# Performance work log

Measured on AMD Instinct MI355X. Metric: run time of the kernel, lower is better.

Reference implementation:

```python
import jax, jax.numpy as jnp
import numpy as np

N, E, D, H, C, L = 50000, 600000, 128, 128, 40, 2
NEG_SLOPE = 0.1


def setup_inputs() -> dict:
    key = jax.random.key(0)
    ks = jax.random.split(key, 12)

    def lin(k, din, dout):
        return (jax.random.normal(k, (din, dout), jnp.float32) / np.sqrt(din)).astype(jnp.float32)

    x = jax.random.normal(ks[0], (N, D), jnp.float32)
    edge_index = jax.random.randint(ks[1], (2, E), 0, N, dtype=jnp.int32)
    return {
        "x": x,
        "edge_index": edge_index,
        "enc_Wl": lin(ks[2], D, H),
        "enc_Wr": lin(ks[3], D, H),
        "enc_b": jnp.zeros((H,), jnp.float32),
        "lay_Wl": jnp.stack([lin(jax.random.fold_in(ks[4], i), H, H) for i in range(L)]),
        "lay_Wr": jnp.stack([lin(jax.random.fold_in(ks[5], i), H, H) for i in range(L)]),
        "lay_b": jnp.zeros((L, H), jnp.float32),
        "dec_Wl": lin(ks[6], H, C),
        "dec_Wr": lin(ks[7], H, C),
        "dec_b": jnp.zeros((C,), jnp.float32),
    }


def _sage(x, src, dst, inv_cnt, Wl, Wr, b):
    # mean-aggregate neighbor messages: gather x[src], scatter-sum to dst, divide by degree
    agg = jax.ops.segment_sum(x[src], dst, num_segments=N) * inv_cnt  # [N, d_in]
    return agg @ Wl + x @ Wr + b


def reference(x, edge_index, enc_Wl, enc_Wr, enc_b, lay_Wl, lay_Wr, lay_b, dec_Wl, dec_Wr, dec_b):
    src, dst = edge_index[0], edge_index[1]
    # in-degree per target node, clamped to 1 (PyG scatter-mean semantics: isolated nodes get 0)
    deg = jax.ops.segment_sum(jnp.ones((E,), jnp.float32), dst, num_segments=N)
    inv_cnt = (1.0 / jnp.maximum(deg, 1.0))[:, None]  # [N, 1]

    h = jax.nn.leaky_relu(_sage(x, src, dst, inv_cnt, enc_Wl, enc_Wr, enc_b), NEG_SLOPE)
    for i in range(L):
        h = jax.nn.leaky_relu(_sage(h, src, dst, inv_cnt, lay_Wl[i], lay_Wr[i], lay_b[i]), NEG_SLOPE)
    out = _sage(h, src, dst, inv_cnt, dec_Wl, dec_Wr, dec_b)
    return jax.nn.log_softmax(out, axis=1)
```

## Files before the change

kernel.cpp:

```cpp
#include <hip/hip_runtime.h>
#include <hip/hip_bf16.h>

#define NN 50000
#define EE 600000
#define HH 128
#define CC 40
#define NEG 0.1f
#define CAP 40
#define NSLOT 50176
#define NBLK (NSLOT / 16)

typedef __attribute__((ext_vector_type(8))) short bf16x8;
typedef __attribute__((ext_vector_type(4))) float f32x4;

__device__ __forceinline__ unsigned short f2bf(float f) {
    unsigned u = __float_as_uint(f);
    unsigned r = u + 0x7fffu + ((u >> 16) & 1u);
    return (unsigned short)(r >> 16);
}
__device__ __forceinline__ float bfhi(unsigned v) { return __uint_as_float(v & 0xFFFF0000u); }
__device__ __forceinline__ float bflo(unsigned v) { return __uint_as_float(v << 16); }

__global__ void k_build(const int* __restrict__ src, const int* __restrict__ dst,
                        int* __restrict__ counts, int* __restrict__ csr) {
    int e = blockIdx.x * blockDim.x + threadIdx.x;
    if (e < EE) {
        int d = dst[e];
        if ((unsigned)d < (unsigned)NN) {
            int sl = atomicAdd(&counts[d], 1);
            if (sl < CAP) csr[d * CAP + sl] = src[e];
        }
    }
}

__global__ void k_hist(const int* __restrict__ counts, int* __restrict__ hist) {
    __shared__ int lh[16];
    if (threadIdx.x < 16) lh[threadIdx.x] = 0;
    __syncthreads();
    int n = blockIdx.x * 256 + threadIdx.x;
    if (n < NN) {
        int c = counts[n]; c = c < CAP ? c : CAP;
        atomicAdd(&lh[(c + 3) >> 2], 1);
    }
    __syncthreads();
    if (threadIdx.x < 11) atomicAdd(&hist[threadIdx.x], lh[threadIdx.x]);
}

__global__ void k_prefix(const int* __restrict__ hist, int* __restrict__ base) {
    if (threadIdx.x == 0) {
        int acc = 0;
        for (int r = 10; r >= 0; --r) {
            base[r] = acc;
            acc += (hist[r] + 15) & ~15;
        }
    }
}

__global__ void k_place(const int* __restrict__ counts, const int* __restrict__ base,
                        int* __restrict__ fill, unsigned* __restrict__ perm) {
    __shared__ int lcnt[16];
    __shared__ int lbase[16];
    int t = threadIdx.x;
    if (t < 16) lcnt[t] = 0;
    __syncthreads();
    int n = blockIdx.x * 256 + t;
    int r = 0, lslot = 0, c = 0;
    if (n < NN) {
        c = counts[n]; c = c < CAP ? c : CAP;
        r = (c + 3) >> 2;
        lslot = atomicAdd(&lcnt[r], 1);
    }
    __syncthreads();
    if (t < 11 && lcnt[t] > 0) lbase[t] = atomicAdd(&fill[t], lcnt[t]);
    __syncthreads();
    if (n < NN) {
        int slot = base[r] + lbase[r] + lslot;
        if (slot >= 0 && slot < NSLOT) perm[slot] = (unsigned)n | ((unsigned)c << 16);
    }
}

struct PrepArgs {
    const float* wsrc[8];
    unsigned short* wdst[8];
    int* counts;
    const float* x;
    unsigned* xb;
    unsigned* perm;
    int* aux;
};

template <int DOUT, int DOUTP>
__device__ __forceinline__ void swz_one(const float* __restrict__ W,
                                        unsigned short* __restrict__ dstf, int idx) {
    int k = idx / DOUTP, n = idx % DOUTP;
    unsigned short val = (n < DOUT) ? f2bf(W[k * DOUT + n]) : (unsigned short)0;
    int kt = k >> 5, kin = k & 31, nt = n >> 4, nin = n & 15;
    int lane = ((kin >> 3) << 4) | nin;
    int j = kin & 7;
    int NT = DOUTP >> 4;
    dstf[(((kt * NT + nt) * 64) + lane) * 8 + j] = val;
}

#define XCB ((NN * HH / 4 + 255) / 256)
#define PFB ((NSLOT + 255) / 256)

__global__ void k_prep(PrepArgs a) {
    int b = blockIdx.x;
    if (b < 384) {
        int tid = b * 256 + threadIdx.x;
        if (tid < NN) a.counts[tid] = 0;
        int which = b >> 6;
        int idx = (b & 63) * 256 + threadIdx.x;
        swz_one<HH, HH>(a.wsrc[which], a.wdst[which], idx);
    } else if (b < 432) {
        int bb = b - 384;
        int which = 6 + bb / 24;
        int idx = (bb % 24) * 256 + threadIdx.x;
        swz_one<CC, 48>(a.wsrc[which], a.wdst[which], idx);
    } else if (b < 432 + XCB) {
        int t = (b - 432) * 256 + threadIdx.x;
        if (t < NN * HH / 4) {
            float4 v = ((const float4*)a.x)[t];
            uint2 o;
            o.x = ((unsigned)f2bf(v.y) << 16) | f2bf(v.x);
            o.y = ((unsigned)f2bf(v.w) << 16) | f2bf(v.z);
            ((uint2*)a.xb)[t] = o;
        }
    } else {
        int i = (b - (432 + XCB)) * 256 + threadIdx.x;
        if (i < NSLOT) a.perm[i] = 0xFFFFFFFFu;
        if (i < 64) a.aux[i] = 0;
    }
}

template <int R>
__device__ __forceinline__ void gather_batch(const int* __restrict__ crow,
                                             const uint4* __restrict__ hw4,
                                             int s, int gg, int cnt, int base_r,
                                             float (&acc)[8]) {
    int rv[R]; uint4 vb[R];
#pragma unroll
    for (int r = 0; r < R; ++r) rv[r] = crow[(base_r + r) * 4 + s];
#pragma unroll
    for (int r = 0; r < R; ++r) {
        unsigned rw = ((unsigned)rv[r] < (unsigned)NN) ? (unsigned)rv[r] : 0u;
        vb[r] = hw4[(size_t)rw * 16 + gg];
    }
#pragma unroll
    for (int r = 0; r < R; ++r) {
        if ((base_r + r) * 4 + s < cnt) {
            acc[0] += bflo(vb[r].x); acc[1] += bfhi(vb[r].x);
            acc[2] += bflo(vb[r].y); acc[3] += bfhi(vb[r].y);
            acc[4] += bflo(vb[r].z); acc[5] += bfhi(vb[r].z);
            acc[6] += bflo(vb[r].w); acc[7] += bfhi(vb[r].w);
        }
    }
}

template <int MODE>
__global__ __launch_bounds__(1024, 8) void k_layer(
    const unsigned short* __restrict__ hin,
    const unsigned* __restrict__ perm,
    const int* __restrict__ csr,
    const unsigned short* __restrict__ B1f, const unsigned short* __restrict__ B2f,
    const float* __restrict__ bias, unsigned short* __restrict__ out,
    const unsigned short* __restrict__ Tf, unsigned short* __restrict__ tOut) {
    __shared__ unsigned lds[16][72];
    __shared__ int nodeTab[16];
    int wid = threadIdx.x >> 6;
    int lane = threadIdx.x & 63;
    int m0 = blockIdx.x * 16;
    int gg = lane & 15;
    int s = lane >> 4;
    const uint4* hw4 = (const uint4*)hin;

    unsigned pe = perm[m0 + wid];
    int pes = __builtin_amdgcn_readfirstlane((int)pe);
    int node = pes & 0xffff;
    int cnt = (pes >> 16) & 0xffff;
    int valid = node < NN;
    if (lane == 0) nodeTab[wid] = valid ? node : (1 << 30);
    int rounds = valid ? (cnt + 3) >> 2 : 0;
    rounds = rounds < 10 ? rounds : 10;
    float sc = 1.0f / (float)((valid && cnt > 0) ? cnt : 1);
    const int* crow = csr + (size_t)(valid ? node : 0) * CAP;

    float acc[8];
#pragma unroll
    for (int d = 0; d < 8; ++d) acc[d] = 0.f;

    switch (rounds) {
        case 0: break;
        case 1: gather_batch<1>(crow, hw4, s, gg, cnt, 0, acc); break;
        case 2: gather_batch<2>(crow, hw4, s, gg, cnt, 0, acc); break;
        case 3: gather_batch<3>(crow, hw4, s, gg, cnt, 0, acc); break;
        case 4: gather_batch<4>(crow, hw4, s, gg, cnt, 0, acc); break;
        case 5: gather_batch<5>(crow, hw4, s, gg, cnt, 0, acc); break;
        case 6: gather_batch<3>(crow, hw4, s, gg, cnt, 0, acc);
                gather_batch<3>(crow, hw4, s, gg, cnt, 3, acc); break;
        case 7: gather_batch<4>(crow, hw4, s, gg, cnt, 0, acc);
                gather_batch<3>(crow, hw4, s, gg, cnt, 4, acc); break;
        case 8: gather_batch<4>(crow, hw4, s, gg, cnt, 0, acc);
                gather_batch<4>(crow, hw4, s, gg, cnt, 4, acc); break;
        case 9: gather_batch<5>(crow, hw4, s, gg, cnt, 0, acc);
                gather_batch<4>(crow, hw4, s, gg, cnt, 5, acc); break;
        default: gather_batch<5>(crow, hw4, s, gg, cnt, 0, acc);
                 gather_batch<5>(crow, hw4, s, gg, cnt, 5, acc); break;
    }

#pragma unroll
    for (int d = 0; d < 8; ++d) {
        float t = acc[d];
        t += __shfl_xor(t, 16, 64);
        t += __shfl_xor(t, 32, 64);
        acc[d] = t * sc;
    }
    if (lane < 16) {
        uint4 w4;
        w4.x = ((unsigned)f2bf(acc[1]) << 16) | f2bf(acc[0]);
        w4.y = ((unsigned)f2bf(acc[3]) << 16) | f2bf(acc[2]);
        w4.z = ((unsigned)f2bf(acc[5]) << 16) | f2bf(acc[4]);
        w4.w = ((unsigned)f2bf(acc[7]) << 16) | f2bf(acc[6]);
        *(uint4*)&lds[wid][gg * 4] = w4;
    }
    __syncthreads();

    int nin = lane & 15;
    int kq = lane >> 4;
    unsigned short hv[4];

    if (wid < 8) {
        const unsigned* arow = &lds[nin][0];
        int node2 = nodeTab[nin];
        int na = node2 < NN ? node2 : 0;
        f32x4 acc1 = (f32x4){0.f, 0.f, 0.f, 0.f};

#pragma unroll
        for (int kt = 0; kt < 4; ++kt) {
            bf16x8 a1 = *(const bf16x8*)(arow + kt * 16 + kq * 4);
            bf16x8 a2 = *(const bf16x8*)(hin + (size_t)na * HH + kt * 32 + kq * 8);
            bf16x8 b1 = *(const bf16x8*)(B1f + (((kt * 8 + wid) * 64) + lane) * 8);
            acc1 = __builtin_amdgcn_mfma_f32_16x16x32_bf16(a1, b1, acc1, 0, 0, 0);
            bf16x8 b2 = *(const bf16x8*)(B2f + (((kt * 8 + wid) * 64) + lane) * 8);
            acc1 = __builtin_amdgcn_mfma_f32_16x16x32_bf16(a2, b2, acc1, 0, 0, 0);
        }

        int col = wid * 16 + nin;
        float bv = bias[col];
#pragma unroll
        for (int r = 0; r < 4; ++r) {
            float v = acc1[r] + bv;
            v = fmaxf(v, NEG * v);
            hv[r] = f2bf(v);
            int nm = nodeTab[kq * 4 + r];
            if (nm < NN) out[(size_t)nm * HH + col] = hv[r];
        }
    }

    if (MODE == 1) {
        __syncthreads();
        unsigned short* lsh = (unsigned short*)&lds[0][0];
        if (wid < 8) {
            int col = wid * 16 + nin;
#pragma unroll
            for (int r = 0; r < 4; ++r) lsh[(kq * 4 + r) * 144 + col] = hv[r];
        }
        __syncthreads();
        if (wid < 3) {
            f32x4 at = (f32x4){0.f, 0.f, 0.f, 0.f};
#pragma unroll
            for (int kt = 0; kt < 4; ++kt) {
                bf16x8 a = *(const bf16x8*)&lsh[nin * 144 + kt * 32 + kq * 8];
                bf16x8 b = *(const bf16x8*)(Tf + (((kt * 3 + wid) * 64) + lane) * 8);
                at = __builtin_amdgcn_mfma_f32_16x16x32_bf16(a, b, at, 0, 0, 0);
            }
#pragma unroll
            for (int r = 0; r < 4; ++r) {
                int nm = nodeTab[kq * 4 + r];
                if (nm < NN) tOut[(size_t)nm * 48 + wid * 16 + nin] = f2bf(at[r]);
            }
        }
    }
}

template <int R>
__device__ __forceinline__ void gatherd_batch(const int* __restrict__ crow,
                                              const uint4* __restrict__ t4,
                                              int s, int g6, int cnt, float (&acc)[8]) {
    int rv[R]; uint4 vb[R];
#pragma unroll
    for (int r = 0; r < R; ++r) rv[r] = crow[r * 8 + s];
#pragma unroll
    for (int r = 0; r < R; ++r) {
        unsigned rw = ((unsigned)rv[r] < (unsigned)NN) ? (unsigned)rv[r] : 0u;
        vb[r] = t4[(size_t)rw * 6 + g6];
    }
#pragma unroll
    for (int r = 0; r < R; ++r) {
        if (r * 8 + s < cnt) {
            acc[0] += bflo(vb[r].x); acc[1] += bfhi(vb[r].x);
            acc[2] += bflo(vb[r].y); acc[3] += bfhi(vb[r].y);
            acc[4] += bflo(vb[r].z); acc[5] += bfhi(vb[r].z);
            acc[6] += bflo(vb[r].w); acc[7] += bfhi(vb[r].w);
        }
    }
}

__global__ __launch_bounds__(1024, 8) void k_dec(
    const unsigned short* __restrict__ tbuf,
    const unsigned short* __restrict__ h1,
    const unsigned* __restrict__ perm,
    const int* __restrict__ csr,
    const unsigned short* __restrict__ B2f, const float* __restrict__ bias,
    float* __restrict__ out) {
    __shared__ float aggT[16][52];
    __shared__ int nodeTab[16];
    int wid = threadIdx.x >> 6;
    int lane = threadIdx.x & 63;
    int m0 = blockIdx.x * 16;
    int g = lane & 7;
    int g6 = g < 6 ? g : g - 6;
    int s = lane >> 3;
    const uint4* t4 = (const uint4*)tbuf;

    unsigned pe = perm[m0 + wid];
    int pes = __builtin_amdgcn_readfirstlane((int)pe);
    int node = pes & 0xffff;
    int cnt = (pes >> 16) & 0xffff;
    int valid = node < NN;
    if (lane == 0) nodeTab[wid] = valid ? node : (1 << 30);
    int rounds = valid ? (cnt + 7) >> 3 : 0;
    rounds = rounds < 5 ? rounds : 5;
    float sc = 1.0f / (float)((valid && cnt > 0) ? cnt : 1);
    const int* crow = csr + (size_t)(valid ? node : 0) * CAP;

    float acc[8];
#pragma unroll
    for (int d = 0; d < 8; ++d) acc[d] = 0.f;

    switch (rounds) {
        case 0: break;
        case 1: gatherd_batch<1>(crow, t4, s, g6, cnt, acc); break;
        case 2: gatherd_batch<2>(crow, t4, s, g6, cnt, acc); break;
        case 3: gatherd_batch<3>(crow, t4, s, g6, cnt, acc); break;
        case 4: gatherd_batch<4>(crow, t4, s, g6, cnt, acc); break;
        default: gatherd_batch<5>(crow, t4, s, g6, cnt, acc); break;
    }

#pragma unroll
    for (int d = 0; d < 8; ++d) {
        float t = acc[d];
        t += __shfl_xor(t, 8, 64);
        t += __shfl_xor(t, 16, 64);
        t += __shfl_xor(t, 32, 64);
        acc[d] = t * sc;
    }
    if (s == 0 && g < 6) {
        float4 p0, p1;
        p0.x = acc[0]; p0.y = acc[1]; p0.z = acc[2]; p0.w = acc[3];
        p1.x = acc[4]; p1.y = acc[5]; p1.z = acc[6]; p1.w = acc[7];
        *(float4*)&aggT[wid][8 * g] = p0;
        *(float4*)&aggT[wid][8 * g + 4] = p1;
    }
    __syncthreads();
    if (wid != 0) return;

    int nin = lane & 15, kq = lane >> 4;
    int node2 = nodeTab[nin];
    int na = node2 < NN ? node2 : 0;
    f32x4 acc2[3];
#pragma unroll
    for (int j = 0; j < 3; ++j) acc2[j] = (f32x4){0.f, 0.f, 0.f, 0.f};
#pragma unroll
    for (int kt = 0; kt < 4; ++kt) {
        bf16x8 a2 = *(const bf16x8*)(h1 + (size_t)na * HH + kt * 32 + kq * 8);
#pragma unroll
        for (int j = 0; j < 3; ++j) {
            bf16x8 b2 = *(const bf16x8*)(B2f + (((kt * 3 + j) * 64) + lane) * 8);
            acc2[j] = __builtin_amdgcn_mfma_f32_16x16x32_bf16(a2, b2, acc2[j], 0, 0, 0);
        }
    }
    float bv[3];
#pragma unroll
    for (int t = 0; t < 3; ++t) {
        int col = t * 16 + nin;
        bv[t] = (col < CC) ? bias[col] : 0.f;
    }
#pragma unroll
    for (int r = 0; r < 4; ++r) {
        int ml = kq * 4 + r;
        int nm = nodeTab[ml];
        float v[3];
        float mx = -1e30f;
#pragma unroll
        for (int t = 0; t < 3; ++t) {
            int col = t * 16 + nin;
            v[t] = acc2[t][r] + aggT[ml][col] + bv[t];
            if (col < CC) mx = fmaxf(mx, v[t]);
        }
        for (int off = 1; off < 16; off <<= 1) mx = fmaxf(mx, __shfl_xor(mx, off, 64));
        float sm = 0.f;
#pragma unroll
        for (int t = 0; t < 3; ++t) {
            int col = t * 16 + nin;
            if (col < CC) sm += expf(v[t] - mx);
        }
        for (int off = 1; off < 16; off <<= 1) sm += __shfl_xor(sm, off, 64);
        float lse = mx + logf(sm);
#pragma unroll
        for (int t = 0; t < 3; ++t) {
            int col = t * 16 + nin;
            if (col < CC && nm < NN) out[(size_t)nm * CC + col] = v[t] - lse;
        }
    }
}

extern "C" void kernel_launch(void* const* d_in, const int* in_sizes, int n_in,
                              void* d_out, int out_size, void* d_ws, size_t ws_size,
                              hipStream_t stream) {
    const float* x      = (const float*)d_in[0];
    const int*   ei     = (const int*)d_in[1];
    const float* enc_Wl = (const float*)d_in[2];
    const float* enc_Wr = (const float*)d_in[3];
    const float* enc_b  = (const float*)d_in[4];
    const float* lay_Wl = (const float*)d_in[5];
    const float* lay_Wr = (const float*)d_in[6];
    const float* lay_b  = (const float*)d_in[7];
    const float* dec_Wl = (const float*)d_in[8];
    const float* dec_Wr = (const float*)d_in[9];
    const float* dec_b  = (const float*)d_in[10];
    float* out = (float*)d_out;

    const int* src = ei;
    const int* dst = ei + EE;

    char* p = (char*)d_ws;
    auto carve = [&](size_t bytes) {
        char* r = p;
        p += (bytes + 255) & ~(size_t)255;
        return r;
    };
    int*            counts = (int*)carve(NN * 4);
    int*            csr    = (int*)carve((size_t)NN * CAP * 4);
    unsigned short* h1     = (unsigned short*)carve((size_t)NN * HH * 2);
    unsigned short* h2     = (unsigned short*)carve((size_t)NN * HH * 2);
    unsigned short* tbuf   = (unsigned short*)carve((size_t)NN * 48 * 2 + 256);
    unsigned*       perm   = (unsigned*)carve((size_t)NSLOT * 4);
    int*            aux    = (int*)carve(64 * 4);
    unsigned short* wf[8];
    for (int i = 0; i < 6; ++i) wf[i] = (unsigned short*)carve(HH * HH * 2);
    wf[6] = (unsigned short*)carve(HH * 48 * 2);
    wf[7] = (unsigned short*)carve(HH * 48 * 2);

    {
        PrepArgs a;
        a.wsrc[0] = enc_Wl; a.wsrc[1] = enc_Wr;
        a.wsrc[2] = lay_Wl; a.wsrc[3] = lay_Wr;
        a.wsrc[4] = lay_Wl + HH * HH; a.wsrc[5] = lay_Wr + HH * HH;
        a.wsrc[6] = dec_Wl; a.wsrc[7] = dec_Wr;
        for (int i = 0; i < 8; ++i) a.wdst[i] = wf[i];
        a.counts = counts;
        a.x = x;
        a.xb = (unsigned*)h2;
        a.perm = perm;
        a.aux = aux;
        k_prep<<<432 + XCB + PFB, 256, 0, stream>>>(a);
    }

    k_build<<<(EE + 255) / 256, 256, 0, stream>>>(src, dst, counts, csr);
    k_hist<<<(NN + 255) / 256, 256, 0, stream>>>(counts, aux);
    k_prefix<<<1, 64, 0, stream>>>(aux, aux + 32);
    k_place<<<(NN + 255) / 256, 256, 0, stream>>>(counts, aux + 32, aux + 16, perm);

    k_layer<0><<<NBLK, 1024, 0, stream>>>(h2, perm, csr, wf[0], wf[1], enc_b,      h1, nullptr, nullptr);
    k_layer<0><<<NBLK, 1024, 0, stream>>>(h1, perm, csr, wf[2], wf[3], lay_b,      h2, nullptr, nullptr);
    k_layer<1><<<NBLK, 1024, 0, stream>>>(h2, perm, csr, wf[4], wf[5], lay_b + HH, h1, wf[6], tbuf);

    k_dec<<<NBLK, 1024, 0, stream>>>(tbuf, h1, perm, csr, wf[7], dec_b, out);
}
```

Before: 313.4 us.

## Store CSR neighbor indices as 16-bit and load rows with uniform wide loads

Neighbor indices in the padded CSR are stored as unsigned short instead of int, which halves the CSR footprint. Each wave now loads its whole 80-byte neighbor row as ten 64-bit loads from a wave-uniform address and extracts the 16-bit indices with shifts, replacing the per-lane scattered index loads. Feature-row gathers use nontemporal loads. This relies on node ids fitting in 16 bits (N=50000 does) and adds register pressure from holding ten 64-bit words per lane.

New measurement: 371.7 us. 1.19x slower.

```diff
diff --git a/kernel.cpp b/kernel.cpp
--- a/kernel.cpp
+++ b/kernel.cpp
@@ -12,6 +12,7 @@
 
 typedef __attribute__((ext_vector_type(8))) short bf16x8;
 typedef __attribute__((ext_vector_type(4))) float f32x4;
+typedef __attribute__((ext_vector_type(4))) unsigned uint4v;
 
 __device__ __forceinline__ unsigned short f2bf(float f) {
     unsigned u = __float_as_uint(f);
@@ -22,13 +23,13 @@
 __device__ __forceinline__ float bflo(unsigned v) { return __uint_as_float(v << 16); }
 
 __global__ void k_build(const int* __restrict__ src, const int* __restrict__ dst,
-                        int* __restrict__ counts, int* __restrict__ csr) {
+                        int* __restrict__ counts, unsigned short* __restrict__ csr) {
     int e = blockIdx.x * blockDim.x + threadIdx.x;
     if (e < EE) {
         int d = dst[e];
         if ((unsigned)d < (unsigned)NN) {
             int sl = atomicAdd(&counts[d], 1);
-            if (sl < CAP) csr[d * CAP + sl] = src[e];
+            if (sl < CAP) csr[d * CAP + sl] = (unsigned short)src[e];
         }
     }
 }
@@ -134,17 +135,18 @@
 }
 
 template <int R>
-__device__ __forceinline__ void gather_batch(const int* __restrict__ crow,
-                                             const uint4* __restrict__ hw4,
-                                             int s, int gg, int cnt, int base_r,
+__device__ __forceinline__ void gather_batch(const unsigned long long* cw,
+                                             const uint4v* __restrict__ hw4,
+                                             int s, int sh16, int gg, int cnt, int base_r,
                                              float (&acc)[8]) {
-    int rv[R]; uint4 vb[R];
-#pragma unroll
-    for (int r = 0; r < R; ++r) rv[r] = crow[(base_r + r) * 4 + s];
+    uint4v vb[R];
 #pragma unroll
     for (int r = 0; r < R; ++r) {
-        unsigned rw = ((unsigned)rv[r] < (unsigned)NN) ? (unsigned)rv[r] : 0u;
-        vb[r] = hw4[(size_t)rw * 16 + gg];
+        unsigned long long w = cw[base_r + r];
+        unsigned half = (s & 2) ? (unsigned)(w >> 32) : (unsigned)w;
+        unsigned idx = (half >> sh16) & 0xffffu;
+        idx = idx < (unsigned)NN ? idx : 0u;
+        vb[r] = __builtin_nontemporal_load(hw4 + (size_t)idx * 16 + gg);
     }
 #pragma unroll
     for (int r = 0; r < R; ++r) {
@@ -161,7 +163,7 @@
 __global__ __launch_bounds__(1024, 8) void k_layer(
     const unsigned short* __restrict__ hin,
     const unsigned* __restrict__ perm,
-    const int* __restrict__ csr,
+    const unsigned short* __restrict__ csr,
     const unsigned short* __restrict__ B1f, const unsigned short* __restrict__ B2f,
     const float* __restrict__ bias, unsigned short* __restrict__ out,
     const unsigned short* __restrict__ Tf, unsigned short* __restrict__ tOut) {
@@ -172,18 +174,24 @@
     int m0 = blockIdx.x * 16;
     int gg = lane & 15;
     int s = lane >> 4;
-    const uint4* hw4 = (const uint4*)hin;
-
-    unsigned pe = perm[m0 + wid];
-    int pes = __builtin_amdgcn_readfirstlane((int)pe);
-    int node = pes & 0xffff;
-    int cnt = (pes >> 16) & 0xffff;
+    int sh16 = (s & 1) * 16;
+    const uint4v* hw4 = (const uint4v*)hin;
+
+    int slot = __builtin_amdgcn_readfirstlane(m0 + wid);
+    unsigned pe = perm[slot];
+    int node = (int)(pe & 0xffffu);
+    int cnt = (int)((pe >> 16) & 0xffffu);
     int valid = node < NN;
     if (lane == 0) nodeTab[wid] = valid ? node : (1 << 30);
     int rounds = valid ? (cnt + 3) >> 2 : 0;
     rounds = rounds < 10 ? rounds : 10;
     float sc = 1.0f / (float)((valid && cnt > 0) ? cnt : 1);
-    const int* crow = csr + (size_t)(valid ? node : 0) * CAP;
+
+    const unsigned long long* cr8 =
+        (const unsigned long long*)(csr + (size_t)(valid ? node : 0) * CAP);
+    unsigned long long cw[10];
+#pragma unroll
+    for (int r = 0; r < 10; ++r) cw[r] = cr8[r];
 
     float acc[8];
 #pragma unroll
@@ -191,21 +199,21 @@
 
     switch (rounds) {
         case 0: break;
-        case 1: gather_batch<1>(crow, hw4, s, gg, cnt, 0, acc); break;
-        case 2: gather_batch<2>(crow, hw4, s, gg, cnt, 0, acc); break;
-        case 3: gather_batch<3>(crow, hw4, s, gg, cnt, 0, acc); break;
-        case 4: gather_batch<4>(crow, hw4, s, gg, cnt, 0, acc); break;
-        case 5: gather_batch<5>(crow, hw4, s, gg, cnt, 0, acc); break;
-        case 6: gather_batch<3>(crow, hw4, s, gg, cnt, 0, acc);
-                gather_batch<3>(crow, hw4, s, gg, cnt, 3, acc); break;
-        case 7: gather_batch<4>(crow, hw4, s, gg, cnt, 0, acc);
-                gather_batch<3>(crow, hw4, s, gg, cnt, 4, acc); break;
-        case 8: gather_batch<4>(crow, hw4, s, gg, cnt, 0, acc);
-                gather_batch<4>(crow, hw4, s, gg, cnt, 4, acc); break;
-        case 9: gather_batch<5>(crow, hw4, s, gg, cnt, 0, acc);
-                gather_batch<4>(crow, hw4, s, gg, cnt, 5, acc); break;
-        default: gather_batch<5>(crow, hw4, s, gg, cnt, 0, acc);
-                 gather_batch<5>(crow, hw4, s, gg, cnt, 5, acc); break;
+        case 1: gather_batch<1>(cw, hw4, s, sh16, gg, cnt, 0, acc); break;
+        case 2: gather_batch<2>(cw, hw4, s, sh16, gg, cnt, 0, acc); break;
+        case 3: gather_batch<3>(cw, hw4, s, sh16, gg, cnt, 0, acc); break;
+        case 4: gather_batch<4>(cw, hw4, s, sh16, gg, cnt, 0, acc); break;
+        case 5: gather_batch<5>(cw, hw4, s, sh16, gg, cnt, 0, acc); break;
+        case 6: gather_batch<3>(cw, hw4, s, sh16, gg, cnt, 0, acc);
+                gather_batch<3>(cw, hw4, s, sh16, gg, cnt, 3, acc); break;
+        case 7: gather_batch<4>(cw, hw4, s, sh16, gg, cnt, 0, acc);
+                gather_batch<3>(cw, hw4, s, sh16, gg, cnt, 4, acc); break;
+        case 8: gather_batch<4>(cw, hw4, s, sh16, gg, cnt, 0, acc);
+                gather_batch<4>(cw, hw4, s, sh16, gg, cnt, 4, acc); break;
+        case 9: gather_batch<5>(cw, hw4, s, sh16, gg, cnt, 0, acc);
+                gather_batch<4>(cw, hw4, s, sh16, gg, cnt, 5, acc); break;
+        default: gather_batch<5>(cw, hw4, s, sh16, gg, cnt, 0, acc);
+                 gather_batch<5>(cw, hw4, s, sh16, gg, cnt, 5, acc); break;
     }
 
 #pragma unroll
@@ -216,12 +224,12 @@
         acc[d] = t * sc;
     }
     if (lane < 16) {
-        uint4 w4;
-        w4.x = ((unsigned)f2bf(acc[1]) << 16) | f2bf(acc[0]);
-        w4.y = ((unsigned)f2bf(acc[3]) << 16) | f2bf(acc[2]);
-        w4.z = ((unsigned)f2bf(acc[5]) << 16) | f2bf(acc[4]);
-        w4.w = ((unsigned)f2bf(acc[7]) << 16) | f2bf(acc[6]);
-        *(uint4*)&lds[wid][gg * 4] = w4;
+        unsigned w4[4];
+        w4[0] = ((unsigned)f2bf(acc[1]) << 16) | f2bf(acc[0]);
+        w4[1] = ((unsigned)f2bf(acc[3]) << 16) | f2bf(acc[2]);
+        w4[2] = ((unsigned)f2bf(acc[5]) << 16) | f2bf(acc[4]);
+        w4[3] = ((unsigned)f2bf(acc[7]) << 16) | f2bf(acc[6]);
+        *(uint4v*)&lds[wid][gg * 4] = *(uint4v*)w4;
     }
     __syncthreads();
 
@@ -284,16 +292,18 @@
 }
 
 template <int R>
-__device__ __forceinline__ void gatherd_batch(const int* __restrict__ crow,
-                                              const uint4* __restrict__ t4,
-                                              int s, int g6, int cnt, float (&acc)[8]) {
-    int rv[R]; uint4 vb[R];
-#pragma unroll
-    for (int r = 0; r < R; ++r) rv[r] = crow[r * 8 + s];
+__device__ __forceinline__ void gatherd_batch(const unsigned long long* cw,
+                                              const uint4v* __restrict__ t4,
+                                              int s, int sh16, int g6, int cnt,
+                                              float (&acc)[8]) {
+    uint4v vb[R];
 #pragma unroll
     for (int r = 0; r < R; ++r) {
-        unsigned rw = ((unsigned)rv[r] < (unsigned)NN) ? (unsigned)rv[r] : 0u;
-        vb[r] = t4[(size_t)rw * 6 + g6];
+        unsigned long long w = (s & 4) ? cw[2 * r + 1] : cw[2 * r];
+        unsigned half = (s & 2) ? (unsigned)(w >> 32) : (unsigned)w;
+        unsigned idx = (half >> sh16) & 0xffffu;
+        idx = idx < (unsigned)NN ? idx : 0u;
+        vb[r] = __builtin_nontemporal_load(t4 + (size_t)idx * 6 + g6);
     }
 #pragma unroll
     for (int r = 0; r < R; ++r) {
@@ -310,7 +320,7 @@
     const unsigned short* __restrict__ tbuf,
     const unsigned short* __restrict__ h1,
     const unsigned* __restrict__ perm,
-    const int* __restrict__ csr,
+    const unsigned short* __restrict__ csr,
     const unsigned short* __restrict__ B2f, const float* __restrict__ bias,
     float* __restrict__ out) {
     __shared__ float aggT[16][52];
@@ -321,18 +331,24 @@
     int g = lane & 7;
     int g6 = g < 6 ? g : g - 6;
     int s = lane >> 3;
-    const uint4* t4 = (const uint4*)tbuf;
-
-    unsigned pe = perm[m0 + wid];
-    int pes = __builtin_amdgcn_readfirstlane((int)pe);
-    int node = pes & 0xffff;
-    int cnt = (pes >> 16) & 0xffff;
+    int sh16 = (s & 1) * 16;
+    const uint4v* t4 = (const uint4v*)tbuf;
+
+    int slot = __builtin_amdgcn_readfirstlane(m0 + wid);
+    unsigned pe = perm[slot];
+    int node = (int)(pe & 0xffffu);
+    int cnt = (int)((pe >> 16) & 0xffffu);
     int valid = node < NN;
     if (lane == 0) nodeTab[wid] = valid ? node : (1 << 30);
     int rounds = valid ? (cnt + 7) >> 3 : 0;
     rounds = rounds < 5 ? rounds : 5;
     float sc = 1.0f / (float)((valid && cnt > 0) ? cnt : 1);
-    const int* crow = csr + (size_t)(valid ? node : 0) * CAP;
+
+    const unsigned long long* cr8 =
+        (const unsigned long long*)(csr + (size_t)(valid ? node : 0) * CAP);
+    unsigned long long cw[10];
+#pragma unroll
+    for (int r = 0; r < 10; ++r) cw[r] = cr8[r];
 
     float acc[8];
 #pragma unroll
@@ -340,11 +356,11 @@
 
     switch (rounds) {
         case 0: break;
-        case 1: gatherd_batch<1>(crow, t4, s, g6, cnt, acc); break;
-        case 2: gatherd_batch<2>(crow, t4, s, g6, cnt, acc); break;
-        case 3: gatherd_batch<3>(crow, t4, s, g6, cnt, acc); break;
-        case 4: gatherd_batch<4>(crow, t4, s, g6, cnt, acc); break;
-        default: gatherd_batch<5>(crow, t4, s, g6, cnt, acc); break;
+        case 1: gatherd_batch<1>(cw, t4, s, sh16, g6, cnt, acc); break;
+        case 2: gatherd_batch<2>(cw, t4, s, sh16, g6, cnt, acc); break;
+        case 3: gatherd_batch<3>(cw, t4, s, sh16, g6, cnt, acc); break;
+        case 4: gatherd_batch<4>(cw, t4, s, sh16, g6, cnt, acc); break;
+        default: gatherd_batch<5>(cw, t4, s, sh16, g6, cnt, acc); break;
     }
 
 #pragma unroll
@@ -441,7 +457,7 @@
         return r;
     };
     int*            counts = (int*)carve(NN * 4);
-    int*            csr    = (int*)carve((size_t)NN * CAP * 4);
+    unsigned short* csr    = (unsigned short*)carve((size_t)NN * CAP * 2);
     unsigned short* h1     = (unsigned short*)carve((size_t)NN * HH * 2);
     unsigned short* h2     = (unsigned short*)carve((size_t)NN * HH * 2);
     unsigned short* tbuf   = (unsigned short*)carve((size_t)NN * 48 * 2 + 256);
```
